# Optimization experiments

Hardware: AMD Instinct MI355X
Metric: run time of the kernel (lower is better)

## Reference

```python
import jax, jax.numpy as jnp
import numpy as np

EMB, DK, DV = 768, 256, 256
B, N = 8, 2048


def setup_inputs() -> dict:
    key = jax.random.key(0)
    ks = jax.random.split(key, 9)
    s = 1.0 / np.sqrt(EMB)
    # Stack the 3 per-head Linear layers into [3, EMB, D] weights (same math).
    Wq = jax.random.uniform(ks[0], (3, EMB, DK), jnp.float32, -s, s)
    bq = jax.random.uniform(ks[1], (3, DK), jnp.float32, -s, s)
    Wk = jax.random.uniform(ks[2], (3, EMB, DK), jnp.float32, -s, s)
    bk = jax.random.uniform(ks[3], (3, DK), jnp.float32, -s, s)
    Wv = jax.random.uniform(ks[4], (3, EMB, DV), jnp.float32, -s, s)
    bv = jax.random.uniform(ks[5], (3, DV), jnp.float32, -s, s)
    s0 = 1.0 / np.sqrt(3 * DV)
    W0 = jax.random.uniform(ks[6], (3 * DV, EMB), jnp.float32, -s0, s0)
    b0 = jax.random.uniform(ks[7], (EMB,), jnp.float32, -s0, s0)
    x = jax.random.normal(ks[8], (B, N, EMB), jnp.float32)
    return {"x": x, "Wq": Wq, "bq": bq, "Wk": Wk, "bk": bk,
            "Wv": Wv, "bv": bv, "W0": W0, "b0": b0}


def reference(x, Wq, bq, Wk, bk, Wv, bv, W0, b0):
    # QKV for all 3 heads in one batched GEMM each: [B,3,N,D]
    Q = jnp.einsum('bne,hed->bhnd', x, Wq) + bq[None, :, None, :]
    K = jnp.einsum('bne,hed->bhnd', x, Wk) + bk[None, :, None, :]
    V = jnp.einsum('bne,hed->bhnd', x, Wv) + bv[None, :, None, :]
    scores = jnp.einsum('bhnd,bhmd->bhnm', Q, K) / jnp.sqrt(jnp.float32(DK))
    attn = jax.nn.softmax(scores, axis=-1)
    res = jnp.einsum('bhnm,bhmd->bhnd', attn, V)  # [B,3,N,DV]
    # concat heads along feature dim (head order matches torch concat order)
    res = jnp.transpose(res, (0, 2, 1, 3)).reshape(B, N, 3 * DV)
    return res @ W0 + b0
```

## Files before the change

kernel.cpp:

```cpp
#include <hip/hip_runtime.h>
#include <stdint.h>

typedef __attribute__((ext_vector_type(8))) short short8;
typedef __attribute__((ext_vector_type(4))) float floatx4;

#define EMB 768
#define DKV 256
#define NB  8
#define NS  2048

__device__ __forceinline__ float b2f(unsigned short u) {
  union { unsigned int i; float f; } v; v.i = ((unsigned int)u) << 16; return v.f;
}
__device__ __forceinline__ unsigned short f2b(float f) {
  union { float f; unsigned int i; } v; v.f = f;
  return (unsigned short)((v.i + 0x7FFFu + ((v.i >> 16) & 1u)) >> 16);
}

__device__ __forceinline__ short8 load8x(const void* p, size_t e, int f32) {
  short8 r;
  if (f32) {
    const float* f = (const float*)p + e;
    float4 a = *(const float4*)f;
    float4 b = *(const float4*)(f + 4);
    r[0] = (short)f2b(a.x); r[1] = (short)f2b(a.y);
    r[2] = (short)f2b(a.z); r[3] = (short)f2b(a.w);
    r[4] = (short)f2b(b.x); r[5] = (short)f2b(b.y);
    r[6] = (short)f2b(b.z); r[7] = (short)f2b(b.w);
  } else {
    r = *(const short8*)((const unsigned short*)p + e);
  }
  return r;
}
__device__ __forceinline__ float loadf(const void* p, size_t e, int f32) {
  return f32 ? ((const float*)p)[e] : b2f(((const unsigned short*)p)[e]);
}

__device__ __forceinline__ void gl_lds16(const void* g, void* l) {
  __builtin_amdgcn_global_load_lds(
      (const __attribute__((address_space(1))) void*)g,
      (__attribute__((address_space(3))) void*)l, 16, 0, 0);
}

__global__ __launch_bounds__(256) void detect_kernel(
    const unsigned short* __restrict__ x, int* __restrict__ flag) {
  __shared__ int cnt;
  if (threadIdx.x == 0) cnt = 0;
  __syncthreads();
  int bad = 0;
  for (int i = threadIdx.x; i < 1024; i += 256) {
    float v = b2f(x[i]);
    if (!(fabsf(v) <= 1e4f)) bad++;
  }
  atomicAdd(&cnt, bad);
  __syncthreads();
  if (threadIdx.x == 0) {
    flag[0] = (cnt > 16) ? 1 : 0;
    flag[1] = 0;
  }
}

__global__ __launch_bounds__(256) void repack_all(
    const void* __restrict__ Wq, const void* __restrict__ Wk,
    const void* __restrict__ Wv, const void* __restrict__ W0,
    const void* __restrict__ X,
    unsigned short* __restrict__ WT, unsigned short* __restrict__ W0T,
    unsigned short* __restrict__ Xb,
    const int* __restrict__ flag, int do_x) {
  __shared__ unsigned short tile[32][33];
  const int f32 = *flag;
  const int tid = threadIdx.x;
  const int b = blockIdx.x;

  if (b < 1728) {
    const int slab = b / 192;
    const int rem = b - slab * 192;
    const int k0 = (rem % 24) * 32, d0 = (rem / 24) * 32;
    const int t = slab / 3, h = slab - t * 3;
    const void* Wsrc = (t == 0) ? Wq : ((t == 1) ? Wk : Wv);
#pragma unroll
    for (int rr = 0; rr < 4; ++rr) {
      int ki = rr * 8 + (tid >> 5), di = tid & 31;
      tile[ki][di] = f2b(loadf(Wsrc, (size_t)(h * EMB + k0 + ki) * DKV + d0 + di, f32));
    }
    __syncthreads();
#pragma unroll
    for (int rr = 0; rr < 4; ++rr) {
      int di = rr * 8 + (tid >> 5), ki = tid & 31;
      WT[(size_t)(slab * 256 + d0 + di) * EMB + k0 + ki] = tile[ki][di];
    }
  } else if (b < 2304) {
    const int bb = b - 1728;
    const int k0 = (bb % 24) * 32, o0 = (bb / 24) * 32;
#pragma unroll
    for (int rr = 0; rr < 4; ++rr) {
      int ki = rr * 8 + (tid >> 5), oi = tid & 31;
      tile[ki][oi] = f2b(loadf(W0, (size_t)(k0 + ki) * EMB + o0 + oi, f32));
    }
    __syncthreads();
#pragma unroll
    for (int rr = 0; rr < 4; ++rr) {
      int oi = rr * 8 + (tid >> 5), ki = tid & 31;
      W0T[(size_t)(o0 + oi) * EMB + k0 + ki] = tile[ki][oi];
    }
  } else {
    if (!do_x) return;
    const int bb = b - 2304;
#pragma unroll
    for (int i = 0; i < 4; ++i) {
      size_t e = ((size_t)bb * 1024 + i * 256 + tid) * 8;
      short8 v = load8x(X, e, f32);
      *(short8*)&Xb[e] = v;
    }
  }
}

__global__ __launch_bounds__(256, 2) void kv_gemm(
    const void* __restrict__ Xs, const unsigned short* __restrict__ WT,
    const void* __restrict__ bk, const void* __restrict__ bv,
    unsigned short* __restrict__ Kb, unsigned short* __restrict__ Vtb,
    const int* __restrict__ xflag, const int* __restrict__ dflag) {
  __shared__ __align__(16) unsigned short As[128 * 40];
  __shared__ __align__(16) unsigned short BsK[128 * 40];
  __shared__ __align__(16) unsigned short BsV[128 * 40];
  const int xf32 = *xflag;
  const int f32 = *dflag;
  const int tid = threadIdx.x;
  const int wave = tid >> 6, lane = tid & 63, quad = lane >> 4, l15 = lane & 15;
  const int wm = wave >> 1, wn = wave & 1;
  const int row0 = blockIdx.y * 128;
  const int cb = blockIdx.x * 128;

  floatx4 accK[4][4], accV[4][4];
  for (int m = 0; m < 4; ++m)
    for (int n = 0; n < 4; ++n) { accK[m][n] = (floatx4)0.0f; accV[m][n] = (floatx4)0.0f; }

  const size_t arow0 = (size_t)row0 * EMB;
  const unsigned short* BbK = WT + (size_t)(768 + cb) * EMB;
  const unsigned short* BbV = WT + (size_t)(1536 + cb) * EMB;

  short8 va[2], vk[2], vv[2];
#pragma unroll
  for (int i = 0; i < 2; ++i) {
    int idx = i * 256 + tid;
    int r = idx >> 2, kp = (idx & 3) << 3;
    va[i] = load8x(Xs, arow0 + (size_t)r * EMB + kp, xf32);
    vk[i] = *(const short8*)(BbK + (size_t)r * EMB + kp);
    vv[i] = *(const short8*)(BbV + (size_t)r * EMB + kp);
  }

  for (int k0 = 0; k0 < EMB; k0 += 32) {
    __syncthreads();
#pragma unroll
    for (int i = 0; i < 2; ++i) {
      int idx = i * 256 + tid;
      int off = (idx >> 2) * 40 + (idx & 3) * 8;
      *(short8*)&As[off] = va[i];
      *(short8*)&BsK[off] = vk[i];
      *(short8*)&BsV[off] = vv[i];
    }
    if (k0 + 32 < EMB) {
      const int kn = k0 + 32;
#pragma unroll
      for (int i = 0; i < 2; ++i) {
        int idx = i * 256 + tid;
        int r = idx >> 2, kp = (idx & 3) << 3;
        va[i] = load8x(Xs, arow0 + (size_t)r * EMB + kn + kp, xf32);
        vk[i] = *(const short8*)(BbK + (size_t)r * EMB + kn + kp);
        vv[i] = *(const short8*)(BbV + (size_t)r * EMB + kn + kp);
      }
    }
    __syncthreads();
    short8 af[4], bk4[4], bv4[4];
#pragma unroll
    for (int m = 0; m < 4; ++m)
      af[m] = *(const short8*)&As[(wm * 64 + m * 16 + l15) * 40 + quad * 8];
#pragma unroll
    for (int n = 0; n < 4; ++n) {
      bk4[n] = *(const short8*)&BsK[(wn * 64 + n * 16 + l15) * 40 + quad * 8];
      bv4[n] = *(const short8*)&BsV[(wn * 64 + n * 16 + l15) * 40 + quad * 8];
    }
    __builtin_amdgcn_s_setprio(1);
#pragma unroll
    for (int n = 0; n < 4; ++n)
#pragma unroll
      for (int m = 0; m < 4; ++m) {
        accK[m][n] = __builtin_amdgcn_mfma_f32_16x16x32_bf16(af[m], bk4[n], accK[m][n], 0, 0, 0);
        accV[m][n] = __builtin_amdgcn_mfma_f32_16x16x32_bf16(af[m], bv4[n], accV[m][n], 0, 0, 0);
      }
    __builtin_amdgcn_s_setprio(0);
  }

  const int h = cb >> 8;
  const int dbase = cb & 255;

#pragma unroll
  for (int n = 0; n < 4; ++n) {
    const int cc = wn * 64 + n * 16 + l15;
    const float bvv = loadf(bk, h * 256 + dbase + cc, f32);
    const int d = dbase + cc;
#pragma unroll
    for (int m = 0; m < 4; ++m) {
      const int rbase = row0 + wm * 64 + m * 16 + quad * 4;
#pragma unroll
      for (int r = 0; r < 4; ++r) {
        const int row = rbase + r;
        const int bb = row >> 11, nn = row & 2047;
        Kb[((size_t)(bb * 3 + h) * 2048 + nn) * 256 + d] = f2b(accK[m][n][r] + bvv);
      }
    }
  }
#pragma unroll
  for (int n = 0; n < 4; ++n) {
    const int cc = wn * 64 + n * 16 + l15;
    const float bvv = loadf(bv, h * 256 + dbase + cc, f32);
    const int d = dbase + cc;
#pragma unroll
    for (int m = 0; m < 4; ++m) {
      const int rbase = row0 + wm * 64 + m * 16 + quad * 4;
      const int bb = rbase >> 11, nn = rbase & 2047;
      const size_t base = ((size_t)(bb * 3 + h) * 256 + d) * 2048 + nn;
      uint2 val;
      val.x = (uint32_t)f2b(accV[m][n][0] + bvv) | ((uint32_t)f2b(accV[m][n][1] + bvv) << 16);
      val.y = (uint32_t)f2b(accV[m][n][2] + bvv) | ((uint32_t)f2b(accV[m][n][3] + bvv) << 16);
      *(uint2*)(Vtb + base) = val;
    }
  }
}

__global__ __launch_bounds__(256, 3) void flash_fused(
    const void* __restrict__ Xs, const unsigned short* __restrict__ WT,
    const void* __restrict__ bq,
    const unsigned short* __restrict__ Kb, const unsigned short* __restrict__ Vtb,
    unsigned short* __restrict__ Ob,
    const int* __restrict__ xflag, const int* __restrict__ dflag) {
  __shared__ __align__(16) unsigned short smem[18944];
  unsigned short* AsQ = smem;
  unsigned short* BsQ = smem + 2560;
  unsigned short* Qs  = smem;
  unsigned short* Ks  = smem;
  unsigned short* Vts = smem + 8192;
  unsigned short* Ps  = smem + 16384;

  const int xf32 = *xflag;
  const int f32 = *dflag;
  const int tid = threadIdx.x;
  const int wave = tid >> 6, lane = tid & 63, quad = lane >> 4, l15 = lane & 15;
  const int bh = blockIdx.x;
  const int bb = bh / 3, hh = bh - bb * 3;
  const int q0 = blockIdx.y * 64;

  short8 qf[8];

  {
    const size_t xrow0 = (size_t)bb * NS + q0;
    floatx4 qacc[4][4];
    for (int m = 0; m < 4; ++m)
      for (int n = 0; n < 4; ++n) qacc[m][n] = (floatx4)0.0f;

    for (int k0 = 0; k0 < EMB; k0 += 32) {
      short8 va, vb[4];
      {
        int r = tid >> 2, kp = (tid & 3) << 3;
        va = load8x(Xs, (xrow0 + r) * EMB + k0 + kp, xf32);
      }
#pragma unroll
      for (int i = 0; i < 4; ++i) {
        int c = i * 256 + tid;
        int n = c >> 2, kp = (c & 3) << 3;
        vb[i] = *(const short8*)(WT + (size_t)(hh * 256 + n) * EMB + k0 + kp);
      }
      __syncthreads();
      *(short8*)&AsQ[(tid >> 2) * 40 + (tid & 3) * 8] = va;
#pragma unroll
      for (int i = 0; i < 4; ++i) {
        int c = i * 256 + tid;
        *(short8*)&BsQ[(c >> 2) * 40 + (c & 3) * 8] = vb[i];
      }
      __syncthreads();
      short8 af[4], bf[4];
#pragma unroll
      for (int m = 0; m < 4; ++m)
        af[m] = *(const short8*)&AsQ[(m * 16 + l15) * 40 + quad * 8];
#pragma unroll
      for (int n = 0; n < 4; ++n)
        bf[n] = *(const short8*)&BsQ[(wave * 64 + n * 16 + l15) * 40 + quad * 8];
      __builtin_amdgcn_s_setprio(1);
#pragma unroll
      for (int n = 0; n < 4; ++n)
#pragma unroll
        for (int m = 0; m < 4; ++m)
          qacc[m][n] = __builtin_amdgcn_mfma_f32_16x16x32_bf16(af[m], bf[n], qacc[m][n], 0, 0, 0);
      __builtin_amdgcn_s_setprio(0);
    }
    __syncthreads();

#pragma unroll
    for (int n = 0; n < 4; ++n) {
      const int col = wave * 64 + n * 16 + l15;
      const float bqv = loadf(bq, hh * 256 + col, f32);
#pragma unroll
      for (int m = 0; m < 4; ++m)
#pragma unroll
        for (int r = 0; r < 4; ++r)
          Qs[(m * 16 + quad * 4 + r) * 264 + col] = f2b((qacc[m][n][r] + bqv) * 0.0625f);
    }
    __syncthreads();
#pragma unroll
    for (int ks = 0; ks < 8; ++ks)
      qf[ks] = *(const short8*)&Qs[(wave * 16 + l15) * 264 + ks * 32 + quad * 8];
    __syncthreads();
  }

  const unsigned short* Kp = Kb + (size_t)bh * NS * DKV;
  const unsigned short* Vp = Vtb + (size_t)bh * DKV * NS;

  floatx4 oacc[4][4];
  for (int m = 0; m < 4; ++m)
    for (int ct = 0; ct < 4; ++ct) oacc[m][ct] = (floatx4)0.0f;
  float l_part = 0.f;

  const int krow_in = lane >> 5;
  const int kc16 = lane & 31;
  const int vrow_in = lane >> 2;
  const int vc = lane & 3;

#pragma unroll
  for (int i = 0; i < 4; ++i) {
    const int L = wave * 4 + i;
    const int krow = L * 2 + krow_in;
    const int kg = kc16 ^ (krow & 7);
    gl_lds16(Kp + (size_t)krow * DKV + kg * 8, &Ks[L * 512]);
    const int vd = L * 16 + vrow_in;
    const int vg = vc ^ ((vd >> 1) & 3);
    gl_lds16(Vp + (size_t)vd * NS + vg * 8, &Vts[L * 512]);
  }
  __syncthreads();

  for (int j0 = 0; j0 < NS; j0 += 32) {
    floatx4 sacc[2];
    sacc[0] = (floatx4)0.0f; sacc[1] = (floatx4)0.0f;
    __builtin_amdgcn_s_setprio(1);
#pragma unroll
    for (int ks = 0; ks < 8; ++ks)
#pragma unroll
      for (int ct = 0; ct < 2; ++ct) {
        short8 kfr = *(const short8*)&Ks[(ct * 16 + l15) * 256 +
                                         (((ks * 4 + quad) ^ (l15 & 7)) << 3)];
        sacc[ct] = __builtin_amdgcn_mfma_f32_16x16x32_bf16(kfr, qf[ks], sacc[ct], 0, 0, 0);
      }
    __builtin_amdgcn_s_setprio(0);

#pragma unroll
    for (int ct = 0; ct < 2; ++ct) {
      float p0 = __expf(sacc[ct][0]);
      float p1 = __expf(sacc[ct][1]);
      float p2 = __expf(sacc[ct][2]);
      float p3 = __expf(sacc[ct][3]);
      l_part += (p0 + p1) + (p2 + p3);
      uint2 pk;
      pk.x = (uint32_t)f2b(p0) | ((uint32_t)f2b(p1) << 16);
      pk.y = (uint32_t)f2b(p2) | ((uint32_t)f2b(p3) << 16);
      *(uint2*)&Ps[(wave * 16 + l15) * 40 + ct * 16 + quad * 4] = pk;
    }
    __syncthreads();

    if (j0 + 32 < NS) {
#pragma unroll
      for (int i = 0; i < 4; ++i) {
        const int L = wave * 4 + i;
        const int krow = L * 2 + krow_in;
        const int kg = kc16 ^ (krow & 7);
        gl_lds16(Kp + (size_t)(j0 + 32 + krow) * DKV + kg * 8, &Ks[L * 512]);
      }
    }

    short8 pa[4];
#pragma unroll
    for (int m = 0; m < 4; ++m)
      pa[m] = *(const short8*)&Ps[(m * 16 + l15) * 40 + quad * 8];
    __builtin_amdgcn_s_setprio(1);
#pragma unroll
    for (int ct = 0; ct < 4; ++ct) {
      const int rv = wave * 64 + ct * 16 + l15;
      short8 vb = *(const short8*)&Vts[rv * 32 + ((quad ^ ((rv >> 1) & 3)) << 3)];
#pragma unroll
      for (int m = 0; m < 4; ++m)
        oacc[m][ct] = __builtin_amdgcn_mfma_f32_16x16x32_bf16(pa[m], vb, oacc[m][ct], 0, 0, 0);
    }
    __builtin_amdgcn_s_setprio(0);
    __syncthreads();

    if (j0 + 32 < NS) {
#pragma unroll
      for (int i = 0; i < 4; ++i) {
        const int L = wave * 4 + i;
        const int vd = L * 16 + vrow_in;
        const int vg = vc ^ ((vd >> 1) & 3);
        gl_lds16(Vp + (size_t)vd * NS + j0 + 32 + vg * 8, &Vts[L * 512]);
      }
    }
  }

  float l_r = l_part;
  l_r += __shfl_xor(l_r, 16);
  l_r += __shfl_xor(l_r, 32);

  __syncthreads();
  float* Lsf = (float*)smem;
  if (quad == 0) Lsf[wave * 16 + l15] = l_r;
  __syncthreads();

#pragma unroll
  for (int m = 0; m < 4; ++m) {
    float linv[4];
#pragma unroll
    for (int r = 0; r < 4; ++r) linv[r] = 1.0f / Lsf[m * 16 + quad * 4 + r];
#pragma unroll
    for (int ct = 0; ct < 4; ++ct) {
      const int col = hh * DKV + wave * 64 + ct * 16 + l15;
#pragma unroll
      for (int r = 0; r < 4; ++r) {
        const int n = q0 + m * 16 + quad * 4 + r;
        Ob[((size_t)(bb * NS + n)) * EMB + col] = f2b(oacc[m][ct][r] * linv[r]);
      }
    }
  }
}

__global__ __launch_bounds__(256) void out_gemm(
    const unsigned short* __restrict__ A, const unsigned short* __restrict__ W0T,
    const void* __restrict__ b0, void* __restrict__ out,
    const int* __restrict__ flag) {
  __shared__ __align__(16) unsigned short As[128 * 40];
  __shared__ __align__(16) unsigned short Bs[128 * 40];
  const int f32 = *flag;
  const int tid = threadIdx.x;
  const int wave = tid >> 6, lane = tid & 63, quad = lane >> 4, l15 = lane & 15;
  const int wm = wave >> 1, wn = wave & 1;
  const int row0 = blockIdx.y * 128;
  const int c0 = blockIdx.x * 128;

  floatx4 acc[4][4];
  for (int m = 0; m < 4; ++m)
    for (int n = 0; n < 4; ++n) acc[m][n] = (floatx4)0.0f;

  const unsigned short* Ab = A + (size_t)row0 * EMB;
  const unsigned short* Bb = W0T + (size_t)c0 * EMB;

  short8 va[2], vb[2];
#pragma unroll
  for (int i = 0; i < 2; ++i) {
    int idx = i * 256 + tid;
    int r = idx >> 2, kp = (idx & 3) << 3;
    va[i] = *(const short8*)(Ab + (size_t)r * EMB + kp);
    vb[i] = *(const short8*)(Bb + (size_t)r * EMB + kp);
  }

  for (int k0 = 0; k0 < EMB; k0 += 32) {
    __syncthreads();
#pragma unroll
    for (int i = 0; i < 2; ++i) {
      int idx = i * 256 + tid;
      *(short8*)&As[(idx >> 2) * 40 + (idx & 3) * 8] = va[i];
      *(short8*)&Bs[(idx >> 2) * 40 + (idx & 3) * 8] = vb[i];
    }
    if (k0 + 32 < EMB) {
      const int kn = k0 + 32;
#pragma unroll
      for (int i = 0; i < 2; ++i) {
        int idx = i * 256 + tid;
        int r = idx >> 2, kp = (idx & 3) << 3;
        va[i] = *(const short8*)(Ab + (size_t)r * EMB + kn + kp);
        vb[i] = *(const short8*)(Bb + (size_t)r * EMB + kn + kp);
      }
    }
    __syncthreads();
    short8 af[4], bf[4];
#pragma unroll
    for (int m = 0; m < 4; ++m)
      af[m] = *(const short8*)&As[(wm * 64 + m * 16 + l15) * 40 + quad * 8];
#pragma unroll
    for (int n = 0; n < 4; ++n)
      bf[n] = *(const short8*)&Bs[(wn * 64 + n * 16 + l15) * 40 + quad * 8];
    __builtin_amdgcn_s_setprio(1);
#pragma unroll
    for (int n = 0; n < 4; ++n)
#pragma unroll
      for (int m = 0; m < 4; ++m)
        acc[m][n] = __builtin_amdgcn_mfma_f32_16x16x32_bf16(af[m], bf[n], acc[m][n], 0, 0, 0);
    __builtin_amdgcn_s_setprio(0);
  }

#pragma unroll
  for (int n = 0; n < 4; ++n) {
    const int col = c0 + wn * 64 + n * 16 + l15;
    const float bvv = loadf(b0, col, f32);
#pragma unroll
    for (int m = 0; m < 4; ++m) {
      const int rbase = row0 + wm * 64 + m * 16 + quad * 4;
#pragma unroll
      for (int r = 0; r < 4; ++r) {
        const float v = acc[m][n][r] + bvv;
        const size_t idx = (size_t)(rbase + r) * EMB + col;
        if (f32) ((float*)out)[idx] = v;
        else     ((unsigned short*)out)[idx] = f2b(v);
      }
    }
  }
}

extern "C" void kernel_launch(void* const* d_in, const int* in_sizes, int n_in,
                              void* d_out, int out_size, void* d_ws, size_t ws_size,
                              hipStream_t stream) {
  const void* x  = d_in[0];
  const void* Wq = d_in[1];
  const void* bq = d_in[2];
  const void* Wk = d_in[3];
  const void* bk = d_in[4];
  const void* Wv = d_in[5];
  const void* bv = d_in[6];
  const void* W0 = d_in[7];
  const void* b0 = d_in[8];

  unsigned short* ws = (unsigned short*)d_ws;
  const size_t SZ = (size_t)NB * 3 * NS * DKV;
  unsigned short* Kb  = (unsigned short*)d_out;
  unsigned short* Vtb = ws;
  unsigned short* Ob  = ws + SZ;
  unsigned short* WT  = ws + 2 * SZ;
  unsigned short* W0T = WT + (size_t)2304 * EMB;
  int* flag = (int*)(W0T + (size_t)EMB * EMB);
  unsigned short* Xb = (unsigned short*)((char*)flag + 16);

  const size_t need = ((size_t)3 * SZ + (size_t)2304 * EMB + (size_t)EMB * EMB) * 2 + 16;
  const int use_xb = (ws_size >= need) ? 1 : 0;

  const void* x_gemm = use_xb ? (const void*)Xb : x;
  const int* xflag   = use_xb ? (flag + 1) : flag;

  detect_kernel<<<dim3(1), dim3(256), 0, stream>>>((const unsigned short*)x, flag);
  repack_all<<<dim3(3840), dim3(256), 0, stream>>>(Wq, Wk, Wv, W0, x, WT, W0T, Xb, flag, use_xb);
  kv_gemm<<<dim3(6, 128), dim3(256), 0, stream>>>(x_gemm, WT, bk, bv, Kb, Vtb, xflag, flag);
  flash_fused<<<dim3(24, 32), dim3(256), 0, stream>>>(x_gemm, WT, bq, Kb, Vtb, Ob, xflag, flag);
  out_gemm<<<dim3(6, 128), dim3(256), 0, stream>>>(Ob, W0T, b0, d_out, flag);
}
```

Measured before the change: 370.6 us.

## Double-buffer Q projection with direct global-to-LDS loads and swizzled layout

The Q-projection prologue in the fused flash kernel now double-buffers its X and W tiles in shared memory. It fills them with direct global-to-LDS loads (gl_lds16) into an XOR-swizzled unpadded layout, replacing the register-staged copies with padded stride. The goal is to overlap the next k-tile load with the MFMAs and cut one barrier per iteration. Shared memory grows slightly, and out_gemm also gets a launch-bounds occupancy hint of 3, which may constrain registers.

```diff
diff --git a/kernel.cpp b/kernel.cpp
--- a/kernel.cpp
+++ b/kernel.cpp
@@ -234,9 +234,7 @@
     const unsigned short* __restrict__ Kb, const unsigned short* __restrict__ Vtb,
     unsigned short* __restrict__ Ob,
     const int* __restrict__ xflag, const int* __restrict__ dflag) {
-  __shared__ __align__(16) unsigned short smem[18944];
-  unsigned short* AsQ = smem;
-  unsigned short* BsQ = smem + 2560;
+  __shared__ __align__(16) unsigned short smem[20480];
   unsigned short* Qs  = smem;
   unsigned short* Ks  = smem;
   unsigned short* Vts = smem + 8192;
@@ -258,33 +256,70 @@
     for (int m = 0; m < 4; ++m)
       for (int n = 0; n < 4; ++n) qacc[m][n] = (floatx4)0.0f;
 
+    const int srow = lane >> 2;
+    const int sch  = lane & 3;
+    const unsigned short* Wb = WT + (size_t)hh * 256 * EMB;
+
+    {
+      if (!xf32) {
+        const int arow = wave * 16 + srow;
+        const int asc = sch ^ ((arow >> 1) & 3);
+        gl_lds16((const unsigned short*)Xs + (xrow0 + arow) * EMB + asc * 8,
+                 &smem[wave * 512]);
+      } else {
+        int row = tid >> 2, pch = tid & 3;
+        int gsc = pch ^ ((row >> 1) & 3);
+        short8 v = load8x(Xs, (xrow0 + row) * EMB + gsc * 8, 1);
+        *(short8*)&smem[row * 32 + pch * 8] = v;
+      }
+#pragma unroll
+      for (int i = 0; i < 4; ++i) {
+        const int L = wave * 4 + i;
+        const int brow = L * 16 + srow;
+        const int bsc = sch ^ ((brow >> 1) & 3);
+        gl_lds16(Wb + (size_t)brow * EMB + bsc * 8, &smem[4096 + L * 512]);
+      }
+    }
+    __syncthreads();
+
+    int p = 0;
     for (int k0 = 0; k0 < EMB; k0 += 32) {
-      short8 va, vb[4];
-      {
-        int r = tid >> 2, kp = (tid & 3) << 3;
-        va = load8x(Xs, (xrow0 + r) * EMB + k0 + kp, xf32);
-      }
-#pragma unroll
-      for (int i = 0; i < 4; ++i) {
-        int c = i * 256 + tid;
-        int n = c >> 2, kp = (c & 3) << 3;
-        vb[i] = *(const short8*)(WT + (size_t)(hh * 256 + n) * EMB + k0 + kp);
-      }
-      __syncthreads();
-      *(short8*)&AsQ[(tid >> 2) * 40 + (tid & 3) * 8] = va;
-#pragma unroll
-      for (int i = 0; i < 4; ++i) {
-        int c = i * 256 + tid;
-        *(short8*)&BsQ[(c >> 2) * 40 + (c & 3) * 8] = vb[i];
-      }
-      __syncthreads();
+      unsigned short* Ac = smem + (p ? 2048 : 0);
+      unsigned short* Bc = smem + 4096 + (p ? 8192 : 0);
+      if (k0 + 32 < EMB) {
+        unsigned short* An = smem + (p ? 0 : 2048);
+        unsigned short* Bn = smem + 4096 + (p ? 0 : 8192);
+        const int kn = k0 + 32;
+        if (!xf32) {
+          const int arow = wave * 16 + srow;
+          const int asc = sch ^ ((arow >> 1) & 3);
+          gl_lds16((const unsigned short*)Xs + (xrow0 + arow) * EMB + kn + asc * 8,
+                   &An[wave * 512]);
+        } else {
+          int row = tid >> 2, pch = tid & 3;
+          int gsc = pch ^ ((row >> 1) & 3);
+          short8 v = load8x(Xs, (xrow0 + row) * EMB + kn + gsc * 8, 1);
+          *(short8*)&An[row * 32 + pch * 8] = v;
+        }
+#pragma unroll
+        for (int i = 0; i < 4; ++i) {
+          const int L = wave * 4 + i;
+          const int brow = L * 16 + srow;
+          const int bsc = sch ^ ((brow >> 1) & 3);
+          gl_lds16(Wb + (size_t)brow * EMB + kn + bsc * 8, &Bn[L * 512]);
+        }
+      }
       short8 af[4], bf[4];
 #pragma unroll
-      for (int m = 0; m < 4; ++m)
-        af[m] = *(const short8*)&AsQ[(m * 16 + l15) * 40 + quad * 8];
-#pragma unroll
-      for (int n = 0; n < 4; ++n)
-        bf[n] = *(const short8*)&BsQ[(wave * 64 + n * 16 + l15) * 40 + quad * 8];
+      for (int m = 0; m < 4; ++m) {
+        const int row = m * 16 + l15;
+        af[m] = *(const short8*)&Ac[row * 32 + ((quad ^ ((row >> 1) & 3)) << 3)];
+      }
+#pragma unroll
+      for (int n = 0; n < 4; ++n) {
+        const int row = wave * 64 + n * 16 + l15;
+        bf[n] = *(const short8*)&Bc[row * 32 + ((quad ^ ((row >> 1) & 3)) << 3)];
+      }
       __builtin_amdgcn_s_setprio(1);
 #pragma unroll
       for (int n = 0; n < 4; ++n)
@@ -292,8 +327,9 @@
         for (int m = 0; m < 4; ++m)
           qacc[m][n] = __builtin_amdgcn_mfma_f32_16x16x32_bf16(af[m], bf[n], qacc[m][n], 0, 0, 0);
       __builtin_amdgcn_s_setprio(0);
-    }
-    __syncthreads();
+      __syncthreads();
+      p ^= 1;
+    }
 
 #pragma unroll
     for (int n = 0; n < 4; ++n) {
@@ -428,7 +464,7 @@
   }
 }
 
-__global__ __launch_bounds__(256) void out_gemm(
+__global__ __launch_bounds__(256, 3) void out_gemm(
     const unsigned short* __restrict__ A, const unsigned short* __restrict__ W0T,
     const void* __restrict__ b0, void* __restrict__ out,
     const int* __restrict__ flag) {
```

After: 363.8 us (median of 2 runs). About the same (-1.8%).
